# Optimization experiments

Measured on AMD Instinct MI355X. Metric: run time of the kernel, lower is better.

## Reference

```python
import jax, jax.numpy as jnp
import numpy as np

H = 1024          # hidden_size
NH = 16           # num_attention_heads
HD = H // NH      # head_dim = 64
FF = 4096         # intermediate_size
EPS = 1e-12       # layer_norm_eps
CLAMP = 1e9


def _layer_norm(x, gamma, beta):
    mu = jnp.mean(x, axis=-1, keepdims=True)
    var = jnp.mean(jnp.square(x - mu), axis=-1, keepdims=True)
    return (x - mu) * jax.lax.rsqrt(var + EPS) * gamma + beta


def setup_inputs() -> dict:
    key = jax.random.key(0)
    ks = jax.random.split(key, 12)
    B, S = 4, 2048
    s_h = 1.0 / np.sqrt(H)
    s_f = 1.0 / np.sqrt(FF)
    return {
        "hidden_states": jax.random.normal(ks[0], (B, S, H), jnp.float32),
        "Wq": jax.random.normal(ks[1], (H, H), jnp.float32) * s_h,
        "bq": jnp.zeros((H,), jnp.float32),
        "Wk": jax.random.normal(ks[2], (H, H), jnp.float32) * s_h,
        "bk": jnp.zeros((H,), jnp.float32),
        "Wv": jax.random.normal(ks[3], (H, H), jnp.float32) * s_h,
        "bv": jnp.zeros((H,), jnp.float32),
        "ln1_g": jnp.ones((H,), jnp.float32),
        "ln1_b": jnp.zeros((H,), jnp.float32),
        "W1": jax.random.normal(ks[4], (H, FF), jnp.float32) * s_h,
        "b1": jnp.zeros((FF,), jnp.float32),
        "W2": jax.random.normal(ks[5], (FF, H), jnp.float32) * s_f,
        "b2": jnp.zeros((H,), jnp.float32),
        "ln2_g": jnp.ones((H,), jnp.float32),
        "ln2_b": jnp.zeros((H,), jnp.float32),
    }


def reference(hidden_states, Wq, bq, Wk, bk, Wv, bv, ln1_g, ln1_b,
              W1, b1, W2, b2, ln2_g, ln2_b):
    B, S, _ = hidden_states.shape
    # QKV projections -> [B, NH, S, HD]
    def heads(x):
        return x.reshape(B, S, NH, HD).transpose(0, 2, 1, 3)
    q = heads(hidden_states @ Wq + bq)
    k = heads(hidden_states @ Wk + bk)
    v = heads(hidden_states @ Wv + bv)
    # manual attention: scale, clamp, softmax + 1e-9 epsilon
    scores = jnp.einsum('bhqd,bhkd->bhqk', q, k) / np.sqrt(HD)
    scores = jnp.clip(scores, -CLAMP, CLAMP)
    probs = jax.nn.softmax(scores, axis=-1) + 1e-9
    ctx = jnp.einsum('bhqk,bhkd->bhqd', probs, v)
    ctx = ctx.transpose(0, 2, 1, 3).reshape(B, S, NH * HD)
    # residual + LN (no output projection in this module)
    x = _layer_norm(hidden_states + ctx, ln1_g, ln1_b)
    # FFN with exact gelu + clamp
    inter = jax.nn.gelu(x @ W1 + b1, approximate=False)
    inter = jnp.clip(inter, -CLAMP, CLAMP)
    out = inter @ W2 + b2
    return _layer_norm(out + x, ln2_g, ln2_b)
```

## Files before the change

kernel.cpp:

```cpp
#include <hip/hip_runtime.h>
#include <math.h>


#define H_   1024
#define NH_  16
#define HD_  64
#define FF_  4096
#define S_   2048
#define B_   4
#define BS_  (B_ * S_)

#define EPI_NONE 0
#define EPI_GELU 1
#define EPI_QKV3 2

typedef unsigned short ushort_t;
typedef short v8s __attribute__((ext_vector_type(8)));
typedef float v4f __attribute__((ext_vector_type(4)));
typedef float v16f __attribute__((ext_vector_type(16)));

#define CQ_ 0.18033688011112042f

__device__ __forceinline__ unsigned short f2bf(float f) {
    union { float f; unsigned int u; } v; v.f = f;
    unsigned int u = v.u;
    return (unsigned short)((u + 0x7fffu + ((u >> 16) & 1u)) >> 16);
}
__device__ __forceinline__ float bf2f(unsigned short h) {
    union { unsigned int u; float f; } v; v.u = ((unsigned int)h) << 16;
    return v.f;
}

__device__ __forceinline__ unsigned cvt_pk_bf16(float lo, float hi) {
    unsigned r;
    asm("v_cvt_pk_bf16_f32 %0, %1, %2" : "=v"(r) : "v"(lo), "v"(hi));
    return r;
}
__device__ __forceinline__ void pl32_swap(unsigned &a, unsigned &b) {
    asm("v_permlane32_swap_b32 %0, %1" : "+v"(a), "+v"(b));
}

typedef __attribute__((address_space(1))) void gvoid;
typedef __attribute__((address_space(3))) void lvoid;
__device__ __forceinline__ void async16(const void* g, void* l) {
    __builtin_amdgcn_global_load_lds((gvoid*)g, (lvoid*)l, 16, 0, 0);
}

__global__ __launch_bounds__(256)
void cast_bf16_kernel(const float* __restrict__ x, ushort_t* __restrict__ y)
{
    const size_t i = ((size_t)blockIdx.x * 256 + threadIdx.x) * 4;
    float4 v = *(const float4*)&x[i];
    ushort4 o;
    o.x = f2bf(v.x); o.y = f2bf(v.y); o.z = f2bf(v.z); o.w = f2bf(v.w);
    *(ushort4*)&y[i] = o;
}

__global__ __launch_bounds__(256)
void cast_transpose_kernel(const float* __restrict__ W, ushort_t* __restrict__ Wt,
                           int K, int N)
{
    __shared__ float tile[32][33];
    const int tid = threadIdx.x;
    const int n0 = blockIdx.x * 32, k0 = blockIdx.y * 32;
    const int r  = tid >> 3;
    const int c4 = (tid & 7) * 4;
    float4 v = *(const float4*)&W[(size_t)(k0 + r) * N + n0 + c4];
    tile[r][c4 + 0] = v.x; tile[r][c4 + 1] = v.y;
    tile[r][c4 + 2] = v.z; tile[r][c4 + 3] = v.w;
    __syncthreads();
    ushort4 o;
    o.x = f2bf(tile[c4 + 0][r]); o.y = f2bf(tile[c4 + 1][r]);
    o.z = f2bf(tile[c4 + 2][r]); o.w = f2bf(tile[c4 + 3][r]);
    *(ushort4*)&Wt[(size_t)(n0 + r) * K + k0 + c4] = o;
}

__global__ __launch_bounds__(256)
void concat3_kernel(const float* __restrict__ a, const float* __restrict__ b,
                    const float* __restrict__ c, float* __restrict__ o)
{
    const int i = blockIdx.x * 256 + threadIdx.x;
    o[i] = (i < 1024) ? a[i] : (i < 2048) ? b[i - 1024] : c[i - 2048];
}

template <int EPI>
__global__ __launch_bounds__(256)
void bgemm_kernel(const ushort_t* __restrict__ A, const ushort_t* __restrict__ Bt,
                  const float* __restrict__ bias, void* __restrict__ Cout,
                  int M, int N, int K)
{
    __shared__ ushort_t Atile[128 * 32];
    __shared__ ushort_t Btile[128 * 32];

    const int tid  = threadIdx.x;
    const int wave = tid >> 6;
    const int lane = tid & 63;
    const int ml   = lane & 15;
    const int q8   = lane >> 4;
    const int wm   = wave >> 1, wn = wave & 1;
    const int blockM = blockIdx.y * 128;
    const int blockN = blockIdx.x * 128;

    v4f acc[4][4];
#pragma unroll
    for (int a = 0; a < 4; ++a)
#pragma unroll
        for (int b = 0; b < 4; ++b) acc[a][b] = (v4f)0.f;

    for (int kt = 0; kt < K; kt += 32) {
#pragma unroll
        for (int i = 0; i < 2; ++i) {
            const int chunk = (i * 4 + wave) * 64 + lane;
            const int row = chunk >> 2;
            const int kp  = chunk & 3;
            async16(A  + (size_t)(blockM + row) * K + kt + kp * 8, &Atile[chunk * 8]);
            async16(Bt + (size_t)(blockN + row) * K + kt + kp * 8, &Btile[chunk * 8]);
        }
        __syncthreads();

        v8s af[4], bfr[4];
#pragma unroll
        for (int a = 0; a < 4; ++a)
            af[a] = *(const v8s*)&Atile[(wm * 64 + a * 16 + ml) * 32 + q8 * 8];
#pragma unroll
        for (int b = 0; b < 4; ++b)
            bfr[b] = *(const v8s*)&Btile[(wn * 64 + b * 16 + ml) * 32 + q8 * 8];
#pragma unroll
        for (int a = 0; a < 4; ++a)
#pragma unroll
            for (int b = 0; b < 4; ++b)
                acc[a][b] = __builtin_amdgcn_mfma_f32_16x16x32_bf16(
                    af[a], bfr[b], acc[a][b], 0, 0, 0);
        __syncthreads();
    }

#pragma unroll
    for (int a = 0; a < 4; ++a) {
#pragma unroll
        for (int b = 0; b < 4; ++b) {
            const int n  = blockN + wn * 64 + b * 16 + ml;
            const float bn = bias[n];
            if (EPI == EPI_QKV3) {
                const int nn = n & 1023;
                const int hh = nn >> 6, dd = nn & 63;
                ushort_t* base = (ushort_t*)Cout + (size_t)(n >> 10) * ((size_t)BS_ * H_);
                if (n < 2048) {
                    const float sc = (n < 1024) ? CQ_ : 1.f;
#pragma unroll
                    for (int r = 0; r < 4; ++r) {
                        const int m = blockM + wm * 64 + a * 16 + q8 * 4 + r;
                        base[(((size_t)((m >> 11) * NH_ + hh)) * S_ + (m & 2047)) * HD_ + dd]
                            = f2bf((acc[a][b][r] + bn) * sc);
                    }
                } else {
                    const int m0 = blockM + wm * 64 + a * 16 + q8 * 4;
                    ushort4 pk;
                    pk.x = f2bf(acc[a][b][0] + bn);
                    pk.y = f2bf(acc[a][b][1] + bn);
                    pk.z = f2bf(acc[a][b][2] + bn);
                    pk.w = f2bf(acc[a][b][3] + bn);
                    *(ushort4*)&base[(((size_t)((m0 >> 11) * NH_ + hh)) * HD_ + dd) * S_
                                     + (m0 & 2047)] = pk;
                }
            } else {
#pragma unroll
                for (int r = 0; r < 4; ++r) {
                    const int m = blockM + wm * 64 + a * 16 + q8 * 4 + r;
                    float v = acc[a][b][r] + bn;
                    if (EPI == EPI_GELU) {
                        v = v * 0.5f * (1.f + erff(v * 0.70710678118654752f));
                        v = fminf(fmaxf(v, -1e9f), 1e9f);
                        ((ushort_t*)Cout)[(size_t)m * N + n] = f2bf(v);
                    } else {
                        ((float*)Cout)[(size_t)m * N + n] = v;
                    }
                }
            }
        }
    }
}

__global__ __launch_bounds__(256)
void vsum_kernel(const ushort_t* __restrict__ VT, float* __restrict__ vsum)
{
    const int bh   = blockIdx.x;
    const int tid  = threadIdx.x;
    const int d    = tid >> 2;
    const int part = tid & 3;
    const ushort_t* p = VT + (size_t)bh * HD_ * S_ + (size_t)d * S_ + part * 512;
    float acc = 0.f;
    for (int i = 0; i < 512; i += 4) {
        ushort4 u = *(const ushort4*)&p[i];
        acc += (bf2f(u.x) + bf2f(u.y)) + (bf2f(u.z) + bf2f(u.w));
    }
    acc += __shfl_xor(acc, 1);
    acc += __shfl_xor(acc, 2);
    if (part == 0) vsum[bh * HD_ + d] = acc;
}

__global__ __launch_bounds__(256, 4)
void flash_kernel(const ushort_t* __restrict__ Q, const ushort_t* __restrict__ Kg,
                  const ushort_t* __restrict__ VT, const float* __restrict__ vsum,
                  float* __restrict__ ctx)
{
    __shared__ ushort_t Qs[128 * 64];
    __shared__ ushort_t Ks[64 * 64];
    __shared__ ushort_t Vs[64 * 64];

    int wg = blockIdx.x;
    wg = (wg & 7) * 128 + (wg >> 3);
    const int bh = wg >> 4;
    const int q0 = (wg & 15) * 128;

    const int tid  = threadIdx.x;
    const int wave = tid >> 6;
    const int lane = tid & 63;
    const int m    = lane & 31;
    const int hi   = lane >> 5;

    const ushort_t* Qp = Q  + (size_t)bh * S_ * HD_ + (size_t)q0 * HD_;
    const ushort_t* Kp = Kg + (size_t)bh * S_ * HD_;
    const ushort_t* Vp = VT + (size_t)bh * HD_ * S_;

#pragma unroll
    for (int i = 0; i < 4; ++i) {
        const int ch = i * 256 + tid;
        const int row = ch >> 3, c = ch & 7;
        async16(Qp + (size_t)row * HD_ + ((c ^ (row & 7)) * 8), &Qs[ch * 8]);
    }

    v16f o0 = (v16f)0.f, o1 = (v16f)0.f;
    float lp0 = 0.f, lp1 = 0.f, lp2 = 0.f, lp3 = 0.f;
    v8s qf[4];
    v8s pf[4];

    for (int t = 0; t < S_ / 64; ++t) {
        const int kv0 = t * 64;
        __syncthreads();
#pragma unroll
        for (int i = 0; i < 2; ++i) {
            const int ch = i * 256 + tid;
            const int row = ch >> 3, c = ch & 7;
            async16(Kp + (size_t)(kv0 + row) * HD_ + ((c ^ (row & 7)) * 8),
                    &Ks[ch * 8]);
            async16(Vp + (size_t)row * S_ + kv0 + ((c ^ (row & 7)) * 8),
                    &Vs[ch * 8]);
        }
        __syncthreads();

        if (t == 0) {
            const int qrow = wave * 32 + m;
#pragma unroll
            for (int c = 0; c < 4; ++c)
                qf[c] = *(const v8s*)&Qs[qrow * 64 + (((2 * c + hi) ^ (qrow & 7)) * 8)];
        }

#pragma unroll
        for (int a = 0; a < 2; ++a) {
            v16f z = (v16f)0.f;
            const int krow = a * 32 + m;
#pragma unroll
            for (int c = 0; c < 4; ++c) {
                v8s kf = *(const v8s*)&Ks[krow * 64 + (((2 * c + hi) ^ (m & 7)) * 8)];
                z = __builtin_amdgcn_mfma_f32_32x32x16_bf16(kf, qf[c], z, 0, 0, 0);
            }
            unsigned u[8];
#pragma unroll
            for (int mm = 0; mm < 8; ++mm) {
                const float plo = __builtin_exp2f(z[2 * mm]);
                const float phi = __builtin_exp2f(z[2 * mm + 1]);
                if ((mm & 3) == 0)      lp0 += plo + phi;
                else if ((mm & 3) == 1) lp1 += plo + phi;
                else if ((mm & 3) == 2) lp2 += plo + phi;
                else                    lp3 += plo + phi;
                u[mm] = cvt_pk_bf16(plo, phi);
            }
            pl32_swap(u[0], u[2]); pl32_swap(u[1], u[3]);
            pl32_swap(u[4], u[6]); pl32_swap(u[5], u[7]);
            union { unsigned w[4]; v8s s; } c0, c1;
            c0.w[0] = u[0]; c0.w[1] = u[1]; c0.w[2] = u[2]; c0.w[3] = u[3];
            c1.w[0] = u[4]; c1.w[1] = u[5]; c1.w[2] = u[6]; c1.w[3] = u[7];
            pf[2 * a]     = c0.s;
            pf[2 * a + 1] = c1.s;
        }

#pragma unroll
        for (int c = 0; c < 4; ++c) {
            const int sw = ((2 * c + hi) ^ (m & 7)) * 8;
            v8s vf0 = *(const v8s*)&Vs[m * 64 + sw];
            v8s vf1 = *(const v8s*)&Vs[(32 + m) * 64 + sw];
            o0 = __builtin_amdgcn_mfma_f32_32x32x16_bf16(vf0, pf[c], o0, 0, 0, 0);
            o1 = __builtin_amdgcn_mfma_f32_32x32x16_bf16(vf1, pf[c], o1, 0, 0, 0);
        }
    }

    float l_r = (lp0 + lp1) + (lp2 + lp3);
    l_r += __shfl_xor(l_r, 32);
    const float linv = 1.f / l_r;

    const int bb = bh >> 4, hh = bh & 15;
    const int srow = q0 + wave * 32 + m;
    float* cp = ctx + ((size_t)(bb * S_ + srow)) * H_ + hh * HD_;
#pragma unroll
    for (int g = 0; g < 2; ++g) {
        const v16f& o = g ? o1 : o0;
#pragma unroll
        for (int rq = 0; rq < 4; ++rq) {
            const int d0 = g * 32 + rq * 8 + hi * 4;
            float4 vs4 = *(const float4*)&vsum[bh * HD_ + d0];
            float4 ov;
            ov.x = o[rq * 4 + 0] * linv + 1e-9f * vs4.x;
            ov.y = o[rq * 4 + 1] * linv + 1e-9f * vs4.y;
            ov.z = o[rq * 4 + 2] * linv + 1e-9f * vs4.z;
            ov.w = o[rq * 4 + 3] * linv + 1e-9f * vs4.w;
            *(float4*)&cp[d0] = ov;
        }
    }
}

template <bool WB>
__global__ __launch_bounds__(256)
void add_ln_kernel(const float* __restrict__ A, const float* __restrict__ Bv,
                   const float* __restrict__ gamma, const float* __restrict__ beta,
                   float* __restrict__ out, ushort_t* __restrict__ outb)
{
    const int row = blockIdx.x;
    const int tid = threadIdx.x;
    const float* a = A  + (size_t)row * H_;
    const float* b = Bv + (size_t)row * H_;

    float4 av = *(const float4*)&a[tid * 4];
    float4 bv = *(const float4*)&b[tid * 4];
    float x[4] = { av.x + bv.x, av.y + bv.y, av.z + bv.z, av.w + bv.w };

    float s  = x[0] + x[1] + x[2] + x[3];
    float s2 = x[0]*x[0] + x[1]*x[1] + x[2]*x[2] + x[3]*x[3];
#pragma unroll
    for (int off = 1; off < 64; off <<= 1) {
        s  += __shfl_xor(s,  off);
        s2 += __shfl_xor(s2, off);
    }
    __shared__ float rs[8];
    const int wave = tid >> 6, lane = tid & 63;
    if (lane == 0) { rs[wave] = s; rs[4 + wave] = s2; }
    __syncthreads();
    const float sum  = rs[0] + rs[1] + rs[2] + rs[3];
    const float sum2 = rs[4] + rs[5] + rs[6] + rs[7];
    const float mu   = sum * (1.f / H_);
    const float var  = sum2 * (1.f / H_) - mu * mu;
    const float rstd = rsqrtf(var + 1e-12f);

    float4 gv = *(const float4*)&gamma[tid * 4];
    float4 be = *(const float4*)&beta[tid * 4];
    float4 ov;
    ov.x = (x[0] - mu) * rstd * gv.x + be.x;
    ov.y = (x[1] - mu) * rstd * gv.y + be.y;
    ov.z = (x[2] - mu) * rstd * gv.z + be.z;
    ov.w = (x[3] - mu) * rstd * gv.w + be.w;
    *(float4*)&out[(size_t)row * H_ + tid * 4] = ov;
    if (WB) {
        ushort4 ob;
        ob.x = f2bf(ov.x); ob.y = f2bf(ov.y); ob.z = f2bf(ov.z); ob.w = f2bf(ov.w);
        *(ushort4*)&outb[(size_t)row * H_ + tid * 4] = ob;
    }
}

extern "C" void kernel_launch(void* const* d_in, const int* in_sizes, int n_in,
                              void* d_out, int out_size, void* d_ws, size_t ws_size,
                              hipStream_t stream)
{
    const float* hidden = (const float*)d_in[0];
    const float* Wq     = (const float*)d_in[1];
    const float* bq     = (const float*)d_in[2];
    const float* Wk     = (const float*)d_in[3];
    const float* bk     = (const float*)d_in[4];
    const float* Wv     = (const float*)d_in[5];
    const float* bv     = (const float*)d_in[6];
    const float* ln1_g  = (const float*)d_in[7];
    const float* ln1_b  = (const float*)d_in[8];
    const float* W1     = (const float*)d_in[9];
    const float* b1     = (const float*)d_in[10];
    const float* W2     = (const float*)d_in[11];
    const float* b2     = (const float*)d_in[12];
    const float* ln2_g  = (const float*)d_in[13];
    const float* ln2_b  = (const float*)d_in[14];

    char* ws = (char*)d_ws;
    const size_t MB = 1024 * 1024;
    ushort_t* Xb    = (ushort_t*)(ws + 0);
    ushort_t* x1b   = (ushort_t*)(ws + 0);
    ushort_t* Wqt   = (ushort_t*)(ws + 16 * MB);
    ushort_t* Wkt   = (ushort_t*)(ws + 18 * MB);
    ushort_t* Wvt   = (ushort_t*)(ws + 20 * MB);
    ushort_t* W1t   = (ushort_t*)(ws + 16 * MB);
    ushort_t* W2t   = (ushort_t*)(ws + 24 * MB);
    ushort_t* q     = (ushort_t*)(ws + 32 * MB);
    ushort_t* k     = (ushort_t*)(ws + 48 * MB);
    ushort_t* vt    = (ushort_t*)(ws + 64 * MB);
    float*    ctx   = (float*)(ws + 80 * MB);
    ushort_t* inter = (ushort_t*)(ws + 32 * MB);
    float*    bcat  = (float*)(ws + 96 * MB);
    float*    vsum  = (float*)(ws + 96 * MB + 16384);
    float*    out2  = (float*)(ws + 96 * MB);
    float*    x1    = (float*)(ws + 128 * MB);
    float*    out   = (float*)d_out;

    const dim3 blk(256);

    cast_bf16_kernel<<<dim3(BS_ * H_ / 1024), blk, 0, stream>>>(hidden, Xb);
    cast_transpose_kernel<<<dim3(32, 32),  blk, 0, stream>>>(Wq, Wqt, H_, H_);
    cast_transpose_kernel<<<dim3(32, 32),  blk, 0, stream>>>(Wk, Wkt, H_, H_);
    cast_transpose_kernel<<<dim3(32, 32),  blk, 0, stream>>>(Wv, Wvt, H_, H_);
    cast_transpose_kernel<<<dim3(32, 128), blk, 0, stream>>>(W2, W2t, FF_, H_);
    concat3_kernel<<<dim3(12), blk, 0, stream>>>(bq, bk, bv, bcat);

    bgemm_kernel<EPI_QKV3><<<dim3(24, 64), blk, 0, stream>>>(
        Xb, Wqt, bcat, q, BS_, 3 * H_, H_);

    cast_transpose_kernel<<<dim3(128, 32), blk, 0, stream>>>(W1, W1t, H_, FF_);

    vsum_kernel<<<dim3(B_ * NH_), blk, 0, stream>>>(vt, vsum);

    flash_kernel<<<dim3((S_ / 128) * (B_ * NH_)), blk, 0, stream>>>(q, k, vt, vsum, ctx);

    add_ln_kernel<true><<<dim3(BS_), blk, 0, stream>>>(hidden, ctx, ln1_g, ln1_b, x1, x1b);

    bgemm_kernel<EPI_GELU><<<dim3(32, 64), blk, 0, stream>>>(x1b, W1t, b1, inter, BS_, FF_, H_);

    bgemm_kernel<EPI_NONE><<<dim3(8, 64), blk, 0, stream>>>(inter, W2t, b2, out2, BS_, H_, FF_);

    add_ln_kernel<false><<<dim3(BS_), blk, 0, stream>>>(out2, x1, ln2_g, ln2_b, out, nullptr);
}
```

Measured before the change: 604.1 us.

## Triple-buffer GEMM LDS tiles with async prefetch, XOR swizzle and priority hints

Turns the bf16 GEMM main loop into a three-stage pipeline. Each iteration issues asynchronous global-to-LDS loads two k-tiles ahead and waits on partial vmcnt, so the single full barrier per tile replaces the previous load-then-sync pattern. It also XOR-swizzles the 16-byte chunk placement within each LDS row to cut bank conflicts on fragment reads, and raises wave priority around the MFMA block. LDS use triples, which can lower occupancy, and the hand-placed waitcnt values depend on exactly four async loads per stage.

```diff
diff --git a/kernel.cpp b/kernel.cpp
--- a/kernel.cpp
+++ b/kernel.cpp
@@ -89,8 +89,8 @@
                   const float* __restrict__ bias, void* __restrict__ Cout,
                   int M, int N, int K)
 {
-    __shared__ ushort_t Atile[128 * 32];
-    __shared__ ushort_t Btile[128 * 32];
+    __shared__ ushort_t Atile[3 * 128 * 32];
+    __shared__ ushort_t Btile[3 * 128 * 32];
 
     const int tid  = threadIdx.x;
     const int wave = tid >> 6;
@@ -107,31 +107,66 @@
 #pragma unroll
         for (int b = 0; b < 4; ++b) acc[a][b] = (v4f)0.f;
 
-    for (int kt = 0; kt < K; kt += 32) {
+    auto stage = [&](int buf, int ktile) {
+        const int kt = ktile * 32;
 #pragma unroll
         for (int i = 0; i < 2; ++i) {
-            const int chunk = (i * 4 + wave) * 64 + lane;
+            const int chunk = i * 256 + wave * 64 + lane;
             const int row = chunk >> 2;
-            const int kp  = chunk & 3;
-            async16(A  + (size_t)(blockM + row) * K + kt + kp * 8, &Atile[chunk * 8]);
-            async16(Bt + (size_t)(blockN + row) * K + kt + kp * 8, &Btile[chunk * 8]);
-        }
-        __syncthreads();
-
+            const int kp  = (chunk & 3) ^ (row & 3);
+            async16(A  + (size_t)(blockM + row) * K + kt + kp * 8,
+                    &Atile[buf * 4096 + chunk * 8]);
+            async16(Bt + (size_t)(blockN + row) * K + kt + kp * 8,
+                    &Btile[buf * 4096 + chunk * 8]);
+        }
+    };
+
+    auto compute = [&](int buf) {
         v8s af[4], bfr[4];
 #pragma unroll
-        for (int a = 0; a < 4; ++a)
-            af[a] = *(const v8s*)&Atile[(wm * 64 + a * 16 + ml) * 32 + q8 * 8];
-#pragma unroll
-        for (int b = 0; b < 4; ++b)
-            bfr[b] = *(const v8s*)&Btile[(wn * 64 + b * 16 + ml) * 32 + q8 * 8];
+        for (int a = 0; a < 4; ++a) {
+            const int r = wm * 64 + a * 16 + ml;
+            af[a] = *(const v8s*)&Atile[buf * 4096 + r * 32 + ((q8 ^ (r & 3)) * 8)];
+        }
+#pragma unroll
+        for (int b = 0; b < 4; ++b) {
+            const int r = wn * 64 + b * 16 + ml;
+            bfr[b] = *(const v8s*)&Btile[buf * 4096 + r * 32 + ((q8 ^ (r & 3)) * 8)];
+        }
+        __builtin_amdgcn_s_setprio(1);
 #pragma unroll
         for (int a = 0; a < 4; ++a)
 #pragma unroll
             for (int b = 0; b < 4; ++b)
                 acc[a][b] = __builtin_amdgcn_mfma_f32_16x16x32_bf16(
                     af[a], bfr[b], acc[a][b], 0, 0, 0);
-        __syncthreads();
+        __builtin_amdgcn_s_setprio(0);
+    };
+
+    const int NT = K >> 5;
+
+    stage(0, 0);
+    stage(1, 1);
+    asm volatile("s_waitcnt vmcnt(4)" ::: "memory");
+    __builtin_amdgcn_s_barrier();
+    __builtin_amdgcn_sched_barrier(0);
+
+    int bc = 0, bs = 2;
+    for (int t = 0; t < NT; ++t) {
+        const bool more = (t + 2 < NT);
+        if (more) {
+            stage(bs, t + 2);
+            bs = (bs == 2) ? 0 : bs + 1;
+        }
+        compute(bc);
+        bc = (bc == 2) ? 0 : bc + 1;
+        if (t < NT - 1) {
+            asm volatile("s_waitcnt lgkmcnt(0)" ::: "memory");
+            if (more) asm volatile("s_waitcnt vmcnt(4)" ::: "memory");
+            else      asm volatile("s_waitcnt vmcnt(0)" ::: "memory");
+            __builtin_amdgcn_s_barrier();
+            __builtin_amdgcn_sched_barrier(0);
+        }
     }
 
 #pragma unroll
```

After: 605.2 us. About the same (+0.2%).
